# Kernel optimization log

Hardware: AMD Instinct MI355X
Metric: run time of the kernel (lower is better)

## Reference

```python
import jax, jax.numpy as jnp
import numpy as np

B, S, DIM = 4, 2048, 512
HEADS, DHEAD = 8, 64
INNER = HEADS * DHEAD


def setup_inputs() -> dict:
    key = jax.random.key(0)
    k1, k2, k3, k4 = jax.random.split(key, 4)
    x = jax.random.normal(k1, (B, S, DIM), dtype=jnp.float32)
    W_qkv = jax.random.normal(k2, (DIM, 3 * INNER), dtype=jnp.float32) * (DIM ** -0.5)
    W_out = jax.random.normal(k3, (INNER, DIM), dtype=jnp.float32) * (INNER ** -0.5)
    b_out = jnp.zeros((DIM,), dtype=jnp.float32)
    # learnable log-temperature, initialized to log(dim_head**-0.5)
    log_temp = jnp.asarray(np.log(DHEAD ** -0.5), dtype=jnp.float32)
    return {"x": x, "W_qkv": W_qkv, "log_temp": log_temp, "W_out": W_out, "b_out": b_out}


def reference(x, W_qkv, log_temp, W_out, b_out):
    b, s, _ = x.shape
    qkv = x @ W_qkv  # [b, s, 3*inner]
    q, k, v = jnp.split(qkv, 3, axis=-1)
    # [b, s, inner] -> [b, h, s, d]
    reshape = lambda t: t.reshape(b, s, HEADS, DHEAD).transpose(0, 2, 1, 3)
    q, k, v = reshape(q), reshape(k), reshape(v)
    dots = jnp.einsum("bhid,bhjd->bhij", q, k) * jnp.exp(log_temp)
    mask_value = -jnp.finfo(dots.dtype).max
    eye = jnp.eye(s, dtype=bool)
    dots = jnp.where(eye, mask_value, dots)
    attn = jax.nn.softmax(dots, axis=-1)
    out = jnp.einsum("bhij,bhjd->bhid", attn, v)
    out = out.transpose(0, 2, 1, 3).reshape(b, s, INNER)
    return out @ W_out + b_out
```

## Files before the change

### kernel.cpp

```cpp
#include <hip/hip_runtime.h>
#include <hip/hip_bf16.h>

#define BB 4
#define SS 2048
#define DIMM 512
#define HH 8
#define DD 64
#define NQKV 1536

typedef float  floatx4 __attribute__((ext_vector_type(4)));
typedef short  bf16x8  __attribute__((ext_vector_type(8)));
typedef short  bf16x4  __attribute__((ext_vector_type(4)));

#define MFMA16(A, B, C) __builtin_amdgcn_mfma_f32_16x16x32_bf16(A, B, C, 0, 0, 0)

__device__ __forceinline__ unsigned short f2bf(float f) {
    unsigned int u = __float_as_uint(f);
    u += 0x7FFFu + ((u >> 16) & 1u);
    return (unsigned short)(u >> 16);
}

__device__ __forceinline__ unsigned int f2bf_pk(float lo, float hi) {
    float2 f; f.x = lo; f.y = hi;
    __hip_bfloat162 h = __float22bfloat162_rn(f);
    return *reinterpret_cast<unsigned int*>(&h);
}

__device__ __forceinline__ float fast_exp2(float x) {
#if __has_builtin(__builtin_amdgcn_exp2f)
    return __builtin_amdgcn_exp2f(x);
#else
    return __exp2f(x);
#endif
}

__device__ __forceinline__ void gl_lds16(const void* g, void* l) {
    __builtin_amdgcn_global_load_lds(
        (__attribute__((address_space(1))) void*)g,
        (__attribute__((address_space(3))) void*)l,
        16, 0, 0);
}

__global__ __launch_bounds__(256) void k_prep(
    const float* __restrict__ x, const float* __restrict__ W_qkv,
    const float* __restrict__ W_out,
    unsigned short* __restrict__ xb, unsigned short* __restrict__ Wq_t,
    unsigned short* __restrict__ Wo_t) {
    __shared__ float t[32][33];
    int bid = blockIdx.x, tid = threadIdx.x;
    if (bid < 4096) {
        int i = (bid * 256 + tid) * 4;
        float4 v = *(const float4*)(x + i);
        ushort4 o;
        o.x = f2bf(v.x); o.y = f2bf(v.y); o.z = f2bf(v.z); o.w = f2bf(v.w);
        *(ushort4*)(xb + i) = o;
        return;
    }
    const float* in; unsigned short* out; int R = 512, C, bx, by;
    if (bid < 4864) { in = W_qkv; out = Wq_t; C = 1536; int blk = bid - 4096; bx = blk % 48; by = blk / 48; }
    else            { in = W_out; out = Wo_t; C = 512;  int blk = bid - 4864; bx = blk % 16; by = blk / 16; }
    int tx = tid & 31, ty = tid >> 5;
    int c0 = bx * 32, r0 = by * 32;
    for (int i = 0; i < 4; i++) {
        int r = r0 + ty + i * 8;
        t[ty + i * 8][tx] = in[(size_t)r * C + c0 + tx];
    }
    __syncthreads();
    for (int i = 0; i < 4; i++) {
        int cc = c0 + ty + i * 8;
        out[(size_t)cc * R + r0 + tx] = f2bf(t[tx][ty + i * 8]);
    }
}

__global__ __launch_bounds__(256) void k_gemm_qkv(
    const unsigned short* __restrict__ A,
    const unsigned short* __restrict__ Bt,
    const float* __restrict__ log_temp,
    unsigned short* __restrict__ Qb,
    unsigned short* __restrict__ Kb,
    unsigned short* __restrict__ Vt) {
    __shared__ unsigned short smem[2][128 * 64];
    unsigned short* As = smem[0];
    unsigned short* Bs = smem[1];
    const int K = 512;
    int m0 = blockIdx.x * 128, n0 = blockIdx.y * 128;
    int tid = threadIdx.x;
    int w = tid >> 6, lane = tid & 63;
    int c = lane & 15, q4 = lane >> 4;
    int wm = w >> 1, wn = w & 1;
    float qscale = __expf(log_temp[0]) * 1.44269504f;

    floatx4 acc[4][4] = {};

    for (int k0 = 0; k0 < K; k0 += 64) {
        __syncthreads();
        for (int i = 0; i < 4; i++) {
            int cidx = w * 256 + i * 64 + lane;
            int row = cidx >> 3, cc = cidx & 7;
            int gcc = cc ^ (row & 7);
            gl_lds16(A + (size_t)(m0 + row) * K + k0 + gcc * 8,
                     As + (size_t)(w * 256 + i * 64) * 8);
            gl_lds16(Bt + (size_t)(n0 + row) * K + k0 + gcc * 8,
                     Bs + (size_t)(w * 256 + i * 64) * 8);
        }
        __syncthreads();
        bf16x8 aF[2][4], bF[2][4];
        for (int kh = 0; kh < 2; kh++)
            for (int mt = 0; mt < 4; mt++) {
                int row = wm * 64 + mt * 16 + c;
                aF[kh][mt] = *(const bf16x8*)&As[row * 64 + (((kh * 4 + q4) ^ (row & 7)) * 8)];
            }
        for (int kh = 0; kh < 2; kh++)
            for (int nt = 0; nt < 4; nt++) {
                int row = wn * 64 + nt * 16 + c;
                bF[kh][nt] = *(const bf16x8*)&Bs[row * 64 + (((kh * 4 + q4) ^ (row & 7)) * 8)];
            }
        for (int kh = 0; kh < 2; kh++)
            for (int mt = 0; mt < 4; mt++)
                for (int nt = 0; nt < 4; nt++)
                    acc[mt][nt] = MFMA16(aF[kh][mt], bF[kh][nt], acc[mt][nt]);
    }

    if (n0 < 1024) {
        for (int nt = 0; nt < 4; nt++) {
            int n = n0 + wn * 64 + nt * 16 + c;
            int t = n >> 9, inner = n & 511;
            int h = inner >> 6, d = inner & 63;
            for (int mt = 0; mt < 4; mt++) {
                for (int r = 0; r < 4; r++) {
                    int m = m0 + wm * 64 + mt * 16 + q4 * 4 + r;
                    int b = m >> 11, s = m & 2047;
                    int bh = b * 8 + h;
                    float v = acc[mt][nt][r];
                    if (t == 0)  Qb[((size_t)bh * SS + s) * 64 + d] = f2bf(v * qscale);
                    else         Kb[((size_t)bh * SS + s) * 64 + d] = f2bf(v);
                }
            }
        }
    } else {
        unsigned short* T = &smem[0][0];
        int b = m0 >> 11, s_base = m0 & 2047;
        for (int half = 0; half < 2; half++) {
            __syncthreads();
            if (wn == half) {
                for (int nt = 0; nt < 4; nt++)
                    for (int mt = 0; mt < 4; mt++)
                        for (int r = 0; r < 4; r++)
                            T[(nt * 16 + c) * 136 + wm * 64 + mt * 16 + q4 * 4 + r] =
                                f2bf(acc[mt][nt][r]);
            }
            __syncthreads();
            for (int rr = 0; rr < 4; rr++) {
                int nl = w * 16 + rr * 4 + q4;
                int ml = c * 8;
                bf16x8 v = *(const bf16x8*)&T[nl * 136 + ml];
                int n = n0 + half * 64 + nl;
                int h = (n >> 6) - 16, d = n & 63;
                int bh = b * 8 + h;
                *(bf16x8*)(Vt + ((size_t)bh * 64 + d) * SS + s_base + ml) = v;
            }
        }
    }
}

__global__ __launch_bounds__(512, 4) void k_attn(
    const unsigned short* __restrict__ Qb,
    const unsigned short* __restrict__ Kb,
    const unsigned short* __restrict__ Vt,
    unsigned short* __restrict__ AO) {
    __shared__ unsigned short KVs[2][2][2][64 * 64];
    int q0 = blockIdx.x * 128;
    int h = blockIdx.y, b = blockIdx.z;
    int bh = b * 8 + h;
    int tid = threadIdx.x, w = tid >> 6, lane = tid & 63;
    int wg = w >> 2, wi = w & 3;
    int c = lane & 15, q4 = lane >> 4;

    const unsigned short* Kbase = Kb + (size_t)bh * SS * 64 + (size_t)wg * 1024 * 64;
    const unsigned short* Vbase = Vt + (size_t)bh * 64 * SS;

    bf16x8 qf[2][2];
    for (int mt = 0; mt < 2; mt++) {
        const unsigned short* qp = Qb + ((size_t)bh * SS + q0 + wi * 32 + mt * 16 + c) * 64;
        qf[mt][0] = *(const bf16x8*)(qp + q4 * 8);
        qf[mt][1] = *(const bf16x8*)(qp + 32 + q4 * 8);
    }

    int cidx0 = wi * 128 + lane, cidx1 = cidx0 + 64;
    int row0 = cidx0 >> 3, cc0 = cidx0 & 7;
    int row1 = cidx1 >> 3, cc1 = cidx1 & 7;
    int fk0 = (row0 & 3) | ((row0 >> 1) & 4);
    int fk1 = (row1 & 3) | ((row1 >> 1) & 4);
    const unsigned short* ksrc0 = Kbase + (size_t)row0 * 64 + (cc0 ^ fk0) * 8;
    const unsigned short* ksrc1 = Kbase + (size_t)row1 * 64 + (cc1 ^ fk1) * 8;
    const unsigned short* vsrc0 = Vbase + (size_t)row0 * SS + wg * 1024 + (cc0 ^ (row0 & 7)) * 8;
    const unsigned short* vsrc1 = Vbase + (size_t)row1 * SS + wg * 1024 + (cc1 ^ (row1 & 7)) * 8;
    unsigned short* kdst0 = &KVs[0][wg][0][0] + wi * 1024;
    unsigned short* kdst1 = kdst0 + 512;
    unsigned short* vdst0 = &KVs[1][wg][0][0] + wi * 1024;
    unsigned short* vdst1 = vdst0 + 512;

    gl_lds16(ksrc0, kdst0); gl_lds16(ksrc1, kdst1);
    gl_lds16(vsrc0, vdst0); gl_lds16(vsrc1, vdst1);

    int mask_j0 = (q0 + wi * 32) & ~63;
    int mglob0 = q0 + wi * 32 + c;
    int mglob1 = mglob0 + 16;
    floatx4 oacc[2][4] = {};
    float psum[2] = {0.f, 0.f};

    for (int jt = 0; jt < 16; jt++) {
        int buf = jt & 1;
        int j0 = wg * 1024 + jt * 64;
        __syncthreads();
        if (jt + 1 < 16) {
            int jl = (jt + 1) * 64;
            gl_lds16(ksrc0 + (size_t)jl * 64, kdst0 + (buf ^ 1) * 4096);
            gl_lds16(ksrc1 + (size_t)jl * 64, kdst1 + (buf ^ 1) * 4096);
            gl_lds16(vsrc0 + jl, vdst0 + (buf ^ 1) * 4096);
            gl_lds16(vsrc1 + jl, vdst1 + (buf ^ 1) * 4096);
        }
        bool diag = (j0 == mask_j0);
        const unsigned short* Ksb = &KVs[0][wg][buf][0];
        const unsigned short* Vsb = &KVs[1][wg][buf][0];

        for (int g = 0; g < 2; g++) {
            bf16x8 kf[2][2];
            for (int inner = 0; inner < 2; inner++) {
                int row = g * 32 + ((c >> 2) << 3) + inner * 4 + (c & 3);
                kf[inner][0] = *(const bf16x8*)&Ksb[row * 64 + ((q4 ^ (c & 7)) * 8)];
                kf[inner][1] = *(const bf16x8*)&Ksb[row * 64 + (((4 + q4) ^ (c & 7)) * 8)];
            }
            bf16x8 vf[4];
            for (int dt = 0; dt < 4; dt++) {
                int vrow = dt * 16 + c;
                vf[dt] = *(const bf16x8*)&Vsb[vrow * 64 + (((g * 4 + q4) ^ (c & 7)) * 8)];
            }

            floatx4 sa[2][2];
            for (int mt = 0; mt < 2; mt++)
                for (int inner = 0; inner < 2; inner++) {
                    floatx4 t = {};
                    t = MFMA16(kf[inner][0], qf[mt][0], t);
                    t = MFMA16(kf[inner][1], qf[mt][1], t);
                    sa[mt][inner] = t;
                }

            if (diag) {
                for (int inner = 0; inner < 2; inner++)
                    for (int r = 0; r < 4; r++) {
                        int jg = j0 + g * 32 + q4 * 8 + inner * 4 + r;
                        if (jg == mglob0) sa[0][inner][r] = -1e30f;
                        if (jg == mglob1) sa[1][inner][r] = -1e30f;
                    }
            }

            for (int mt = 0; mt < 2; mt++) {
                float e0 = fast_exp2(sa[mt][0][0]), e1 = fast_exp2(sa[mt][0][1]);
                float e2 = fast_exp2(sa[mt][0][2]), e3 = fast_exp2(sa[mt][0][3]);
                float e4 = fast_exp2(sa[mt][1][0]), e5 = fast_exp2(sa[mt][1][1]);
                float e6 = fast_exp2(sa[mt][1][2]), e7 = fast_exp2(sa[mt][1][3]);
                psum[mt] += ((e0 + e1) + (e2 + e3)) + ((e4 + e5) + (e6 + e7));
                union { bf16x8 v; unsigned int u[4]; } P;
                P.u[0] = f2bf_pk(e0, e1); P.u[1] = f2bf_pk(e2, e3);
                P.u[2] = f2bf_pk(e4, e5); P.u[3] = f2bf_pk(e6, e7);
                for (int dt = 0; dt < 4; dt++)
                    oacc[mt][dt] = MFMA16(P.v, vf[dt], oacc[mt][dt]);
            }
        }
    }

    __syncthreads();
    float* p = (float*)&KVs[0][0][0][0] + ((size_t)(wi * 64 + lane)) * 35;
    if (wg == 1) {
        for (int mt = 0; mt < 2; mt++)
            for (int dt = 0; dt < 4; dt++)
                for (int r = 0; r < 4; r++)
                    p[mt * 16 + dt * 4 + r] = oacc[mt][dt][r];
        p[32] = psum[0]; p[33] = psum[1];
    }
    __syncthreads();
    if (wg == 0) {
        for (int mt = 0; mt < 2; mt++)
            for (int dt = 0; dt < 4; dt++)
                for (int r = 0; r < 4; r++)
                    oacc[mt][dt][r] += p[mt * 16 + dt * 4 + r];
        psum[0] += p[32]; psum[1] += p[33];

        for (int mt = 0; mt < 2; mt++) {
            float l = psum[mt];
            l += __shfl_xor(l, 16);
            l += __shfl_xor(l, 32);
            for (int r = 0; r < 4; r++) {
                float lr = __shfl(l, q4 * 4 + r, 64);
                float inv = 1.0f / lr;
                int s = q0 + wi * 32 + mt * 16 + q4 * 4 + r;
                for (int dt = 0; dt < 4; dt++)
                    AO[((size_t)b * SS + s) * 512 + h * 64 + dt * 16 + c] =
                        f2bf(oacc[mt][dt][r] * inv);
            }
        }
    }
}

__global__ __launch_bounds__(256) void k_gemm_out(
    const unsigned short* __restrict__ A,
    const unsigned short* __restrict__ Bt,
    const float* __restrict__ bias,
    float* __restrict__ out) {
    __shared__ unsigned short As[64 * 64];
    __shared__ unsigned short Bs[128 * 64];
    const int K = 512;
    int m0 = blockIdx.x * 64, n0 = blockIdx.y * 128;
    int tid = threadIdx.x;
    int w = tid >> 6, lane = tid & 63;
    int c = lane & 15, q4 = lane >> 4;

    floatx4 acc[8] = {};

    for (int k0 = 0; k0 < K; k0 += 64) {
        __syncthreads();
        for (int i = 0; i < 2; i++) {
            int cidx = i * 256 + tid;
            int row = cidx >> 3, cc = cidx & 7;
            int gcc = cc ^ (row & 7);
            gl_lds16(A + (size_t)(m0 + row) * K + k0 + gcc * 8,
                     As + (size_t)(i * 256 + w * 64) * 8);
        }
        for (int i = 0; i < 4; i++) {
            int cidx = i * 256 + tid;
            int row = cidx >> 3, cc = cidx & 7;
            int gcc = cc ^ (row & 7);
            gl_lds16(Bt + (size_t)(n0 + row) * K + k0 + gcc * 8,
                     Bs + (size_t)(i * 256 + w * 64) * 8);
        }
        __syncthreads();
        bf16x8 aF[2], bF[2][8];
        for (int kh = 0; kh < 2; kh++) {
            int row = w * 16 + c;
            aF[kh] = *(const bf16x8*)&As[row * 64 + (((kh * 4 + q4) ^ (row & 7)) * 8)];
        }
        for (int kh = 0; kh < 2; kh++)
            for (int nt = 0; nt < 8; nt++) {
                int row = nt * 16 + c;
                bF[kh][nt] = *(const bf16x8*)&Bs[row * 64 + (((kh * 4 + q4) ^ (row & 7)) * 8)];
            }
        for (int kh = 0; kh < 2; kh++)
            for (int nt = 0; nt < 8; nt++)
                acc[nt] = MFMA16(aF[kh], bF[kh][nt], acc[nt]);
    }

    for (int nt = 0; nt < 8; nt++) {
        int n = n0 + nt * 16 + c;
        float bv = bias[n];
        for (int r = 0; r < 4; r++) {
            int m = m0 + w * 16 + q4 * 4 + r;
            out[(size_t)m * 512 + n] = acc[nt][r] + bv;
        }
    }
}

extern "C" void kernel_launch(void* const* d_in, const int* in_sizes, int n_in,
                              void* d_out, int out_size, void* d_ws, size_t ws_size,
                              hipStream_t stream) {
    const float* x        = (const float*)d_in[0];
    const float* W_qkv    = (const float*)d_in[1];
    const float* log_temp = (const float*)d_in[2];
    const float* W_out    = (const float*)d_in[3];
    const float* b_out    = (const float*)d_in[4];
    float* out = (float*)d_out;

    char* ws = (char*)d_ws;
    unsigned short* xb   = (unsigned short*)(ws + 0);
    unsigned short* Wq_t = (unsigned short*)(ws + 8388608);
    unsigned short* Wo_t = (unsigned short*)(ws + 9961472);
    unsigned short* Qb   = (unsigned short*)(ws + 10485760);
    unsigned short* Kb   = (unsigned short*)(ws + 18874368);
    unsigned short* Vt   = (unsigned short*)(ws + 27262976);
    unsigned short* AO   = (unsigned short*)(ws + 35651584);

    k_prep<<<5120, 256, 0, stream>>>(x, W_qkv, W_out, xb, Wq_t, Wo_t);
    k_gemm_qkv<<<dim3(64, 12), 256, 0, stream>>>(xb, Wq_t, log_temp, Qb, Kb, Vt);
    k_attn<<<dim3(16, 8, 4), 512, 0, stream>>>(Qb, Kb, Vt, AO);
    k_gemm_out<<<dim3(128, 4), 256, 0, stream>>>(AO, Wo_t, b_out, out);
}
```

Baseline: 147.1 us.

## Swizzle block order for XCD locality, compute row sums via MFMA, add setprio

Remaps the QKV GEMM and attention blocks to a 1D grid with an XCD-aware swizzle, so that blocks sharing K/V or weight tiles land on the same L2 slice. In attention, the softmax row sum is computed by an extra MFMA against a vector of ones instead of scalar adds and cross-lane shuffles, and MFMA sections are wrapped in s_setprio. The ones-MFMA sums the bf16-rounded probabilities, which changes numerics slightly, and it adds matrix-core work on each tile.

```diff
diff --git a/kernel.cpp b/kernel.cpp
--- a/kernel.cpp
+++ b/kernel.cpp
@@ -83,7 +83,12 @@
     unsigned short* As = smem[0];
     unsigned short* Bs = smem[1];
     const int K = 512;
-    int m0 = blockIdx.x * 128, n0 = blockIdx.y * 128;
+    int bid = blockIdx.x;
+    int swz = (bid & 7) * 96 + (bid >> 3);
+    int local = swz % 96;
+    int m_blk = (swz / 96) * 8 + (local & 7);
+    int n_blk = local >> 3;
+    int m0 = m_blk * 128, n0 = n_blk * 128;
     int tid = threadIdx.x;
     int w = tid >> 6, lane = tid & 63;
     int c = lane & 15, q4 = lane >> 4;
@@ -169,9 +174,11 @@
     const unsigned short* __restrict__ Vt,
     unsigned short* __restrict__ AO) {
     __shared__ unsigned short KVs[2][2][2][64 * 64];
-    int q0 = blockIdx.x * 128;
-    int h = blockIdx.y, b = blockIdx.z;
-    int bh = b * 8 + h;
+    int bid = blockIdx.x;
+    int swz = (bid & 7) * 64 + (bid >> 3);
+    int q0 = (swz & 15) * 128;
+    int bh = swz >> 4;
+    int h = bh & 7, b = bh >> 3;
     int tid = threadIdx.x, w = tid >> 6, lane = tid & 63;
     int wg = w >> 2, wi = w & 3;
     int c = lane & 15, q4 = lane >> 4;
@@ -185,6 +192,8 @@
         qf[mt][0] = *(const bf16x8*)(qp + q4 * 8);
         qf[mt][1] = *(const bf16x8*)(qp + 32 + q4 * 8);
     }
+    bf16x8 ones;
+    for (int i = 0; i < 8; i++) ones[i] = (short)0x3F80;
 
     int cidx0 = wi * 128 + lane, cidx1 = cidx0 + 64;
     int row0 = cidx0 >> 3, cc0 = cidx0 & 7;
@@ -207,7 +216,7 @@
     int mglob0 = q0 + wi * 32 + c;
     int mglob1 = mglob0 + 16;
     floatx4 oacc[2][4] = {};
-    float psum[2] = {0.f, 0.f};
+    floatx4 osum[2] = {};
 
     for (int jt = 0; jt < 16; jt++) {
         int buf = jt & 1;
@@ -238,6 +247,7 @@
             }
 
             floatx4 sa[2][2];
+            __builtin_amdgcn_s_setprio(1);
             for (int mt = 0; mt < 2; mt++)
                 for (int inner = 0; inner < 2; inner++) {
                     floatx4 t = {};
@@ -245,6 +255,7 @@
                     t = MFMA16(kf[inner][1], qf[mt][1], t);
                     sa[mt][inner] = t;
                 }
+            __builtin_amdgcn_s_setprio(0);
 
             if (diag) {
                 for (int inner = 0; inner < 2; inner++)
@@ -260,24 +271,28 @@
                 float e2 = fast_exp2(sa[mt][0][2]), e3 = fast_exp2(sa[mt][0][3]);
                 float e4 = fast_exp2(sa[mt][1][0]), e5 = fast_exp2(sa[mt][1][1]);
                 float e6 = fast_exp2(sa[mt][1][2]), e7 = fast_exp2(sa[mt][1][3]);
-                psum[mt] += ((e0 + e1) + (e2 + e3)) + ((e4 + e5) + (e6 + e7));
                 union { bf16x8 v; unsigned int u[4]; } P;
                 P.u[0] = f2bf_pk(e0, e1); P.u[1] = f2bf_pk(e2, e3);
                 P.u[2] = f2bf_pk(e4, e5); P.u[3] = f2bf_pk(e6, e7);
+                __builtin_amdgcn_s_setprio(1);
                 for (int dt = 0; dt < 4; dt++)
                     oacc[mt][dt] = MFMA16(P.v, vf[dt], oacc[mt][dt]);
+                osum[mt] = MFMA16(P.v, ones, osum[mt]);
+                __builtin_amdgcn_s_setprio(0);
             }
         }
     }
 
     __syncthreads();
-    float* p = (float*)&KVs[0][0][0][0] + ((size_t)(wi * 64 + lane)) * 35;
+    float* p = (float*)&KVs[0][0][0][0] + ((size_t)(wi * 64 + lane)) * 41;
     if (wg == 1) {
         for (int mt = 0; mt < 2; mt++)
             for (int dt = 0; dt < 4; dt++)
                 for (int r = 0; r < 4; r++)
                     p[mt * 16 + dt * 4 + r] = oacc[mt][dt][r];
-        p[32] = psum[0]; p[33] = psum[1];
+        for (int mt = 0; mt < 2; mt++)
+            for (int r = 0; r < 4; r++)
+                p[32 + mt * 4 + r] = osum[mt][r];
     }
     __syncthreads();
     if (wg == 0) {
@@ -285,15 +300,13 @@
             for (int dt = 0; dt < 4; dt++)
                 for (int r = 0; r < 4; r++)
                     oacc[mt][dt][r] += p[mt * 16 + dt * 4 + r];
-        psum[0] += p[32]; psum[1] += p[33];
+        for (int mt = 0; mt < 2; mt++)
+            for (int r = 0; r < 4; r++)
+                osum[mt][r] += p[32 + mt * 4 + r];
 
         for (int mt = 0; mt < 2; mt++) {
-            float l = psum[mt];
-            l += __shfl_xor(l, 16);
-            l += __shfl_xor(l, 32);
             for (int r = 0; r < 4; r++) {
-                float lr = __shfl(l, q4 * 4 + r, 64);
-                float inv = 1.0f / lr;
+                float inv = 1.0f / osum[mt][r];
                 int s = q0 + wi * 32 + mt * 16 + q4 * 4 + r;
                 for (int dt = 0; dt < 4; dt++)
                     AO[((size_t)b * SS + s) * 512 + h * 64 + dt * 16 + c] =
@@ -380,7 +393,7 @@
     unsigned short* AO   = (unsigned short*)(ws + 35651584);
 
     k_prep<<<5120, 256, 0, stream>>>(x, W_qkv, W_out, xb, Wq_t, Wo_t);
-    k_gemm_qkv<<<dim3(64, 12), 256, 0, stream>>>(xb, Wq_t, log_temp, Qb, Kb, Vt);
-    k_attn<<<dim3(16, 8, 4), 512, 0, stream>>>(Qb, Kb, Vt, AO);
+    k_gemm_qkv<<<768, 256, 0, stream>>>(xb, Wq_t, log_temp, Qb, Kb, Vt);
+    k_attn<<<512, 512, 0, stream>>>(Qb, Kb, Vt, AO);
     k_gemm_out<<<dim3(128, 4), 256, 0, stream>>>(AO, Wo_t, b_out, out);
 }
```

Measured after the change: 149.5 us. No clear change (+1.7%).
